# Performance work log

Hardware: AMD Instinct MI355X
Metric: run time of the kernel (lower is better)

The kernel has to match this reference:

```python
import jax, jax.numpy as jnp
import numpy as np

N_USERS = 100000
N_ITEMS = 100000
EMBED_DIM = 64
N_LAYERS = 3
NNZ = 1000000


def setup_inputs() -> dict:
    key = jax.random.key(0)
    k1, k2, k3, k4, k5 = jax.random.split(key, 5)
    N = N_USERS + N_ITEMS
    user_w = jax.random.normal(k1, (N_USERS, EMBED_DIM), dtype=jnp.float32) * 0.1
    item_w = jax.random.normal(k2, (N_ITEMS, EMBED_DIM), dtype=jnp.float32) * 0.1
    vals = jax.random.uniform(k3, (NNZ,), dtype=jnp.float32)
    rows = jax.random.randint(k4, (NNZ,), 0, N, dtype=jnp.int64 if jax.config.jax_enable_x64 else jnp.int32)
    cols = jax.random.randint(k5, (NNZ,), 0, N, dtype=jnp.int64 if jax.config.jax_enable_x64 else jnp.int32)
    return {"user_w": user_w, "item_w": item_w, "vals": vals, "rows": rows, "cols": cols}


def _spmm(vals, rows, cols, x, n):
    # sparse [n,n] COO  @  dense [n,d]  ->  [n,d]
    gathered = vals[:, None] * x[cols]          # [nnz, d]
    return jax.ops.segment_sum(gathered, rows, num_segments=n)


def reference(user_w, item_w, vals, rows, cols):
    # LightGCN-style propagation (SimGCL.propagate, perturb=False)
    n = user_w.shape[0] + item_w.shape[0]
    x = jnp.concatenate([user_w, item_w], axis=0)   # [N, d]
    acc = x                                         # running sum over layer stack
    for _ in range(N_LAYERS):
        x = _spmm(vals, rows, cols, x, n)
        acc = acc + x
    out = acc / jnp.asarray(N_LAYERS + 1, dtype=acc.dtype)  # mean over stacked embs
    return out[: user_w.shape[0]], out[user_w.shape[0]:]
```

## Files before the change

kernel.cpp:

```cpp
#include <hip/hip_runtime.h>
#include <hip/hip_bf16.h>
#include <hip/hip_fp16.h>

#define EMB 64
#define SCAN_CHUNK 1024
#define BSHIFT 11
#define BROWS (1 << BSHIFT)
#define NBMAX 128
#define TILE 4096

__device__ __forceinline__ float ld_elem(const void* p, long long i, int bf) {
    if (bf) return (float)((const __hip_bfloat16*)p)[i];
    return ((const float*)p)[i];
}

__global__ void hist_rows(const int* __restrict__ rows, int* __restrict__ counts, int nnz,
                          const unsigned short* __restrict__ v16, int* __restrict__ flag) {
    int tid = blockIdx.x * blockDim.x + threadIdx.x;
    int stride = gridDim.x * blockDim.x;
    for (int e = tid; e < nnz; e += stride) atomicAdd(&counts[rows[e]], 1);
    if (tid == 0) {
        int hits = 0;
        for (int i = 0; i < 256; ++i) {
            unsigned int hb = v16[i] >> 8;
            unsigned int ex = hb & 0x7F;
            if (hb < 0x80 && ex >= 0x30 && ex < 0x40) hits++;
        }
        *flag = (hits >= 200) ? 1 : 0;
    }
}

__global__ void scan_blocks(const int* __restrict__ in, int* __restrict__ excl,
                            int* __restrict__ blocksums, int n) {
    __shared__ int lds[256];
    int base = blockIdx.x * SCAN_CHUNK;
    int t = threadIdx.x;
    int c[4]; int s = 0;
    for (int k = 0; k < 4; ++k) {
        int i = base + t * 4 + k;
        c[k] = (i < n) ? in[i] : 0;
        s += c[k];
    }
    lds[t] = s;
    __syncthreads();
    for (int off = 1; off < 256; off <<= 1) {
        int v = lds[t];
        int add = (t >= off) ? lds[t - off] : 0;
        __syncthreads();
        lds[t] = v + add;
        __syncthreads();
    }
    int run = (t > 0) ? lds[t - 1] : 0;
    if (t == 255) blocksums[blockIdx.x] = lds[255];
    for (int k = 0; k < 4; ++k) {
        int i = base + t * 4 + k;
        if (i < n) excl[i] = run;
        run += c[k];
    }
}

__global__ void scan_fixup(int* __restrict__ excl, const int* __restrict__ bsums,
                           int* __restrict__ bcur, int n, int nrows, int nb) {
    __shared__ int lds[256];
    int t = threadIdx.x;
    lds[t] = (t < nb) ? bsums[t] : 0;
    __syncthreads();
    for (int off = 1; off < 256; off <<= 1) {
        int v = lds[t];
        int add = (t >= off) ? lds[t - off] : 0;
        __syncthreads();
        lds[t] = v + add;
        __syncthreads();
    }
    __syncthreads();
    int i = blockIdx.x * blockDim.x + threadIdx.x;
    if (i >= n) return;
    int b = i / SCAN_CHUNK;
    int v = excl[i] + (b > 0 ? lds[b - 1] : 0);
    excl[i] = v;
    if (i < nrows && (i & (BROWS - 1)) == 0) bcur[i >> BSHIFT] = v;
}

__global__ void bucket_scatter(const void* __restrict__ vals, const int* __restrict__ rows,
                               const int* __restrict__ cols, int* __restrict__ bcur,
                               float2* __restrict__ staged, int nnz, int nbuck,
                               const int* __restrict__ flagp) {
    __shared__ int hist[NBMAX];
    __shared__ int exb[NBMAX];
    __shared__ int gb[NBMAX];
    __shared__ int sc[NBMAX];
    __shared__ float2 st[TILE];
    __shared__ int bkt[TILE];
    int t = threadIdx.x;
    int bf = *flagp;

    for (int tile = blockIdx.x * TILE; tile < nnz; tile += gridDim.x * TILE) {
        int cnt = min(TILE, nnz - tile);
        for (int i = t; i < NBMAX; i += 256) hist[i] = 0;
        __syncthreads();

        int   myb[16], myo[16], mmeta[16];
        float mv[16];
#pragma unroll
        for (int k = 0; k < 16; ++k) {
            int i = tile + k * 256 + t;
            if (i < nnz && (k * 256 + t) < cnt) {
                int r = rows[i], c = cols[i];
                mv[k]    = ld_elem(vals, i, bf);
                myb[k]   = r >> BSHIFT;
                mmeta[k] = ((r & (BROWS - 1)) << 18) | c;
                myo[k]   = atomicAdd(&hist[myb[k]], 1);
            } else myb[k] = -1;
        }
        __syncthreads();

        if (t < NBMAX) sc[t] = hist[t];
        __syncthreads();
        for (int off = 1; off < NBMAX; off <<= 1) {
            int v = 0;
            if (t < NBMAX) { v = sc[t]; if (t >= off) v += sc[t - off]; }
            __syncthreads();
            if (t < NBMAX) sc[t] = v;
            __syncthreads();
        }
        if (t < NBMAX) {
            exb[t] = sc[t] - hist[t];
            if (t < nbuck && hist[t] > 0) gb[t] = atomicAdd(&bcur[t], hist[t]);
        }
        __syncthreads();

#pragma unroll
        for (int k = 0; k < 16; ++k) {
            if (myb[k] >= 0) {
                int p = exb[myb[k]] + myo[k];
                st[p]  = make_float2(mv[k], __int_as_float(mmeta[k]));
                bkt[p] = myb[k];
            }
        }
        __syncthreads();

        for (int p = t; p < cnt; p += 256) {
            int b = bkt[p];
            staged[gb[b] + (p - exb[b])] = st[p];
        }
        __syncthreads();
    }
}

__global__ void bucket_place(const int* __restrict__ row_ptr,
                             const float2* __restrict__ staged,
                             float2* __restrict__ edges, int nrows) {
    __shared__ int loffs[BROWS];
    int b = blockIdx.x;
    int rlo = b << BSHIFT;
    int rhi = min(rlo + BROWS, nrows);
    int nr  = rhi - rlo;
    int base = row_ptr[rlo];
    int end  = row_ptr[rhi];
    for (int i = threadIdx.x; i < nr; i += 256) loffs[i] = row_ptr[rlo + i] - base;
    __syncthreads();
    for (int p = base + threadIdx.x; p < end; p += 256) {
        float2 rec = staged[p];
        int meta = __float_as_int(rec.y);
        int lr = meta >> 18;
        int c  = meta & 0x3FFFF;
        int pos = atomicAdd(&loffs[lr], 1);
        edges[base + pos] = make_float2(rec.x, __int_as_float(c));
    }
}

__device__ __forceinline__ float4 ld4_x0(const void* uw, const void* iw,
                                         int n_user_elems, long long e, int bf) {
    const void* base = uw;
    if (e >= (long long)n_user_elems) { base = iw; e -= n_user_elems; }
    if (bf) {
        uint2 r = *reinterpret_cast<const uint2*>((const unsigned short*)base + e);
        return make_float4(__uint_as_float((r.x & 0xFFFFu) << 16),
                           __uint_as_float(r.x & 0xFFFF0000u),
                           __uint_as_float((r.y & 0xFFFFu) << 16),
                           __uint_as_float(r.y & 0xFFFF0000u));
    }
    return *reinterpret_cast<const float4*>((const float*)base + e);
}

__device__ __forceinline__ float4 ld4_f16(const __half* g, long long e) {
    uint2 r = *reinterpret_cast<const uint2*>(g + e);
    union { unsigned int u; __half2 h; } c0, c1;
    c0.u = r.x; c1.u = r.y;
    float2 f0 = __half22float2(c0.h), f1 = __half22float2(c1.h);
    return make_float4(f0.x, f0.y, f1.x, f1.y);
}

template <int GMODE, int OMODE>
__global__ void spmm_csr4(const int* __restrict__ row_ptr,
                          const float2* __restrict__ edges,
                          const void* __restrict__ uw, const void* __restrict__ iw,
                          int n_user_elems,
                          const __half* __restrict__ gin, void* __restrict__ gout,
                          int nrows, const int* __restrict__ flagp) {
    int tid  = blockIdx.x * blockDim.x + threadIdx.x;
    int wave = tid >> 6;
    int lane = threadIdx.x & 63;
    int g    = lane >> 4;
    int l    = lane & 15;
    int wid  = wave * 4 + g;
    if (wid >= nrows) return;
    int bf = *flagp;
    int beg = row_ptr[wid], end = row_ptr[wid + 1];
    float a0 = 0.f, a1 = 0.f, a2 = 0.f, a3 = 0.f;

#define GATHER(E, X) { \
        long long ce = (long long)__float_as_int((E).y) * EMB + l * 4; \
        if (GMODE == 0) X = ld4_x0(uw, iw, n_user_elems, ce, bf); \
        else            X = ld4_f16(gin, ce); }
#define ACC(E, X) { a0 += (E).x * (X).x; a1 += (E).x * (X).y; \
                    a2 += (E).x * (X).z; a3 += (E).x * (X).w; }

    int j = beg;
    for (; j + 4 <= end; j += 4) {
        float2 e0 = edges[j], e1 = edges[j + 1], e2 = edges[j + 2], e3 = edges[j + 3];
        float4 xa, xb, xc, xd;
        GATHER(e0, xa); GATHER(e1, xb); GATHER(e2, xc); GATHER(e3, xd);
        ACC(e0, xa); ACC(e1, xb); ACC(e2, xc); ACC(e3, xd);
    }
    if (j + 2 <= end) {
        float2 e0 = edges[j], e1 = edges[j + 1];
        float4 xa, xb;
        GATHER(e0, xa); GATHER(e1, xb);
        ACC(e0, xa); ACC(e1, xb);
        j += 2;
    }
    if (j < end) {
        float2 e0 = edges[j];
        float4 xa; GATHER(e0, xa);
        ACC(e0, xa);
    }
#undef GATHER
#undef ACC

    long long re = (long long)wid * EMB + l * 4;
    float4 x0v = ld4_x0(uw, iw, n_user_elems, re, bf);
    float o0 = x0v.x + a0, o1 = x0v.y + a1, o2 = x0v.z + a2, o3 = x0v.w + a3;

    if (OMODE == 1) {
        __half2 h01 = __floats2half2_rn(o0, o1);
        __half2 h23 = __floats2half2_rn(o2, o3);
        union { __half2 h; unsigned int u; } p0, p1;
        p0.h = h01; p1.h = h23;
        uint2 out; out.x = p0.u; out.y = p1.u;
        reinterpret_cast<uint2*>(gout)[re >> 2] = out;
    } else {
        o0 *= 0.25f; o1 *= 0.25f; o2 *= 0.25f; o3 *= 0.25f;
        if (bf) {
            __hip_bfloat16 b0 = (__hip_bfloat16)o0, b1 = (__hip_bfloat16)o1;
            __hip_bfloat16 b2 = (__hip_bfloat16)o2, b3 = (__hip_bfloat16)o3;
            unsigned short s0 = *reinterpret_cast<unsigned short*>(&b0);
            unsigned short s1 = *reinterpret_cast<unsigned short*>(&b1);
            unsigned short s2 = *reinterpret_cast<unsigned short*>(&b2);
            unsigned short s3 = *reinterpret_cast<unsigned short*>(&b3);
            uint2 out;
            out.x = (unsigned int)s0 | ((unsigned int)s1 << 16);
            out.y = (unsigned int)s2 | ((unsigned int)s3 << 16);
            reinterpret_cast<uint2*>(gout)[re >> 2] = out;
        } else {
            reinterpret_cast<float4*>(gout)[re >> 2] = make_float4(o0, o1, o2, o3);
        }
    }
}

extern "C" void kernel_launch(void* const* d_in, const int* in_sizes, int n_in,
                              void* d_out, int out_size, void* d_ws, size_t ws_size,
                              hipStream_t stream) {
    const void* uw   = d_in[0];
    const void* iw   = d_in[1];
    const void* vals = d_in[2];
    const int*  rows = (const int*)d_in[3];
    const int*  cols = (const int*)d_in[4];

    const int n_user = in_sizes[0];
    const int total  = in_sizes[0] + in_sizes[1];
    const int nnz    = in_sizes[2];
    const int nrows  = total / EMB;
    const int nbuck  = (nrows + BROWS - 1) >> BSHIFT;

    char* p = (char*)d_ws;
    auto alloc = [&](size_t bytes) { char* q = p; p += (bytes + 255) & ~(size_t)255; return q; };
    int*    flag    = (int*)   alloc(sizeof(int));
    int*    row_ptr = (int*)   alloc((size_t)(nrows + 1) * sizeof(int));
    int*    counts  = (int*)   alloc((size_t)(nrows + 1) * sizeof(int));
    int*    bcur    = (int*)   alloc(NBMAX * sizeof(int));
    int*    bsums   = (int*)   alloc(1024 * sizeof(int));
    float2* staged  = (float2*)alloc((size_t)nnz * sizeof(float2));
    float2* edges   = (float2*)alloc((size_t)nnz * sizeof(float2));
    size_t used = (size_t)(p - (char*)d_ws);
    size_t avail = (ws_size > used) ? ws_size - used : 0;

    const size_t g_f16 = (size_t)total * sizeof(__half);
    __half *g2, *g3;
    if (avail >= 2 * g_f16 + 512) { g2 = (__half*)alloc(g_f16); g3 = (__half*)alloc(g_f16); }
    else { g2 = (__half*)d_out; g3 = (__half*)alloc(g_f16); }

    hipMemsetAsync(counts, 0, (size_t)(nrows + 1) * sizeof(int), stream);
    const int hb = (nnz / 4 + 255) / 256;
    hist_rows<<<hb, 256, 0, stream>>>(rows, counts, nnz, (const unsigned short*)vals, flag);
    const int n_scan = nrows + 1;
    const int nb = (n_scan + SCAN_CHUNK - 1) / SCAN_CHUNK;
    scan_blocks<<<nb, 256, 0, stream>>>(counts, row_ptr, bsums, n_scan);
    scan_fixup<<<(n_scan + 255) / 256, 256, 0, stream>>>(row_ptr, bsums, bcur, n_scan, nrows, nb);

    const int ntiles = (nnz + TILE - 1) / TILE;
    bucket_scatter<<<ntiles, 256, 0, stream>>>(vals, rows, cols, bcur, staged, nnz, nbuck, flag);
    bucket_place<<<nbuck, 256, 0, stream>>>(row_ptr, staged, edges, nrows);

    const int nwaves = (nrows + 3) / 4;
    const int rb = (nwaves * 64 + 255) / 256;
    spmm_csr4<0, 1><<<rb, 256, 0, stream>>>(row_ptr, edges, uw, iw, n_user,
                                            nullptr, g2, nrows, flag);
    spmm_csr4<1, 1><<<rb, 256, 0, stream>>>(row_ptr, edges, uw, iw, n_user,
                                            g2, g3, nrows, flag);
    spmm_csr4<1, 3><<<rb, 256, 0, stream>>>(row_ptr, edges, uw, iw, n_user,
                                            g3, d_out, nrows, flag);
}
```

Before: 300.0 us.

## Build CSR from coarse bucket histogram and compute per-row offsets inside buckets

Swaps the per-row global-atomic histogram plus the two-kernel scan for a coarse per-bucket histogram kept in shared memory and a single-block scan. Per-row counts and the row_ptr prefix sum are now computed inside each bucket's block during the placement pass, from the staged metadata. This removes about 1M global atomics, a large memset and two scan launches, but each bucket block now makes two passes over its staged edges and runs a local scan. Only 98 bucket blocks do that work, so the placement stage may not fill the GPU.

New measurement: 272.1 us. -9.3%, faster.

```diff
diff --git a/kernel.cpp b/kernel.cpp
--- a/kernel.cpp
+++ b/kernel.cpp
@@ -3,7 +3,6 @@
 #include <hip/hip_fp16.h>
 
 #define EMB 64
-#define SCAN_CHUNK 1024
 #define BSHIFT 11
 #define BROWS (1 << BSHIFT)
 #define NBMAX 128
@@ -14,11 +13,39 @@
     return ((const float*)p)[i];
 }
 
-__global__ void hist_rows(const int* __restrict__ rows, int* __restrict__ counts, int nnz,
-                          const unsigned short* __restrict__ v16, int* __restrict__ flag) {
-    int tid = blockIdx.x * blockDim.x + threadIdx.x;
+__device__ __forceinline__ float4 ld4_x0(const void* uw, const void* iw,
+                                         int n_user_elems, long long e, int bf) {
+    const void* base = uw;
+    if (e >= (long long)n_user_elems) { base = iw; e -= n_user_elems; }
+    if (bf) {
+        uint2 r = *reinterpret_cast<const uint2*>((const unsigned short*)base + e);
+        return make_float4(__uint_as_float((r.x & 0xFFFFu) << 16),
+                           __uint_as_float(r.x & 0xFFFF0000u),
+                           __uint_as_float((r.y & 0xFFFFu) << 16),
+                           __uint_as_float(r.y & 0xFFFF0000u));
+    }
+    return *reinterpret_cast<const float4*>((const float*)base + e);
+}
+
+__device__ __forceinline__ float4 ld4_f16(const __half* g, long long e) {
+    uint2 r = *reinterpret_cast<const uint2*>(g + e);
+    union { unsigned int u; __half2 h; } c0, c1;
+    c0.u = r.x; c1.u = r.y;
+    float2 f0 = __half22float2(c0.h), f1 = __half22float2(c1.h);
+    return make_float4(f0.x, f0.y, f1.x, f1.y);
+}
+
+__global__ void hist_coarse(const int* __restrict__ rows, int* __restrict__ counts, int nnz,
+                            const unsigned short* __restrict__ v16, int* __restrict__ flag) {
+    __shared__ int h[NBMAX];
+    int t = threadIdx.x;
+    if (t < NBMAX) h[t] = 0;
+    __syncthreads();
+    int tid = blockIdx.x * blockDim.x + t;
     int stride = gridDim.x * blockDim.x;
-    for (int e = tid; e < nnz; e += stride) atomicAdd(&counts[rows[e]], 1);
+    for (int e = tid; e < nnz; e += stride) atomicAdd(&h[rows[e] >> BSHIFT], 1);
+    __syncthreads();
+    if (t < NBMAX) { int v = h[t]; if (v) atomicAdd(&counts[t], v); }
     if (tid == 0) {
         int hits = 0;
         for (int i = 0; i < 256; ++i) {
@@ -30,55 +57,22 @@
     }
 }
 
-__global__ void scan_blocks(const int* __restrict__ in, int* __restrict__ excl,
-                            int* __restrict__ blocksums, int n) {
-    __shared__ int lds[256];
-    int base = blockIdx.x * SCAN_CHUNK;
+__global__ void scan_coarse(const int* __restrict__ counts, int* __restrict__ cptr,
+                            int* __restrict__ bcur, int nb) {
+    __shared__ int lds[128];
     int t = threadIdx.x;
-    int c[4]; int s = 0;
-    for (int k = 0; k < 4; ++k) {
-        int i = base + t * 4 + k;
-        c[k] = (i < n) ? in[i] : 0;
-        s += c[k];
-    }
-    lds[t] = s;
-    __syncthreads();
-    for (int off = 1; off < 256; off <<= 1) {
-        int v = lds[t];
-        int add = (t >= off) ? lds[t - off] : 0;
-        __syncthreads();
-        lds[t] = v + add;
-        __syncthreads();
-    }
-    int run = (t > 0) ? lds[t - 1] : 0;
-    if (t == 255) blocksums[blockIdx.x] = lds[255];
-    for (int k = 0; k < 4; ++k) {
-        int i = base + t * 4 + k;
-        if (i < n) excl[i] = run;
-        run += c[k];
-    }
-}
-
-__global__ void scan_fixup(int* __restrict__ excl, const int* __restrict__ bsums,
-                           int* __restrict__ bcur, int n, int nrows, int nb) {
-    __shared__ int lds[256];
-    int t = threadIdx.x;
-    lds[t] = (t < nb) ? bsums[t] : 0;
-    __syncthreads();
-    for (int off = 1; off < 256; off <<= 1) {
-        int v = lds[t];
-        int add = (t >= off) ? lds[t - off] : 0;
-        __syncthreads();
-        lds[t] = v + add;
-        __syncthreads();
-    }
-    __syncthreads();
-    int i = blockIdx.x * blockDim.x + threadIdx.x;
-    if (i >= n) return;
-    int b = i / SCAN_CHUNK;
-    int v = excl[i] + (b > 0 ? lds[b - 1] : 0);
-    excl[i] = v;
-    if (i < nrows && (i & (BROWS - 1)) == 0) bcur[i >> BSHIFT] = v;
+    int v = (t < nb) ? counts[t] : 0;
+    lds[t] = v;
+    __syncthreads();
+    for (int off = 1; off < 128; off <<= 1) {
+        int x = lds[t];
+        int a = (t >= off) ? lds[t - off] : 0;
+        __syncthreads();
+        lds[t] = x + a;
+        __syncthreads();
+    }
+    if (t < nb) { int excl = lds[t] - v; cptr[t] = excl; bcur[t] = excl; }
+    if (t == 0) cptr[nb] = lds[127];
 }
 
 __global__ void bucket_scatter(const void* __restrict__ vals, const int* __restrict__ rows,
@@ -147,48 +141,57 @@
     }
 }
 
-__global__ void bucket_place(const int* __restrict__ row_ptr,
-                             const float2* __restrict__ staged,
-                             float2* __restrict__ edges, int nrows) {
-    __shared__ int loffs[BROWS];
+__global__ void bucket_csr(const int* __restrict__ cptr,
+                           const float2* __restrict__ staged,
+                           float2* __restrict__ edges,
+                           int* __restrict__ row_ptr, int nrows, int nbuck) {
+    __shared__ int rcnt[BROWS];
+    __shared__ int ssum[256];
     int b = blockIdx.x;
+    int t = threadIdx.x;
+    int cbeg = cptr[b], cend = cptr[b + 1];
     int rlo = b << BSHIFT;
-    int rhi = min(rlo + BROWS, nrows);
-    int nr  = rhi - rlo;
-    int base = row_ptr[rlo];
-    int end  = row_ptr[rhi];
-    for (int i = threadIdx.x; i < nr; i += 256) loffs[i] = row_ptr[rlo + i] - base;
-    __syncthreads();
-    for (int p = base + threadIdx.x; p < end; p += 256) {
-        float2 rec = staged[p];
+    int nr = min(BROWS, nrows - rlo);
+
+    for (int i = t; i < BROWS; i += 256) rcnt[i] = 0;
+    __syncthreads();
+
+    const int* sm = (const int*)staged;
+    for (int i = cbeg + t; i < cend; i += 256) {
+        int lr = (sm[2 * i + 1] >> 18) & (BROWS - 1);
+        atomicAdd(&rcnt[lr], 1);
+    }
+    __syncthreads();
+
+    int base = t * 8;
+    int loc[8]; int s = 0;
+#pragma unroll
+    for (int k = 0; k < 8; ++k) { loc[k] = rcnt[base + k]; s += loc[k]; }
+    ssum[t] = s;
+    __syncthreads();
+    for (int off = 1; off < 256; off <<= 1) {
+        int x = ssum[t];
+        int a = (t >= off) ? ssum[t - off] : 0;
+        __syncthreads();
+        ssum[t] = x + a;
+        __syncthreads();
+    }
+    int run = (t > 0) ? ssum[t - 1] : 0;
+#pragma unroll
+    for (int k = 0; k < 8; ++k) { int c = loc[k]; rcnt[base + k] = run; run += c; }
+    __syncthreads();
+
+    for (int i = t; i < nr; i += 256) row_ptr[rlo + i] = cbeg + rcnt[i];
+    if (b == nbuck - 1 && t == 0) row_ptr[nrows] = cend;
+
+    for (int i = cbeg + t; i < cend; i += 256) {
+        float2 rec = staged[i];
         int meta = __float_as_int(rec.y);
-        int lr = meta >> 18;
+        int lr = (meta >> 18) & (BROWS - 1);
         int c  = meta & 0x3FFFF;
-        int pos = atomicAdd(&loffs[lr], 1);
-        edges[base + pos] = make_float2(rec.x, __int_as_float(c));
-    }
-}
-
-__device__ __forceinline__ float4 ld4_x0(const void* uw, const void* iw,
-                                         int n_user_elems, long long e, int bf) {
-    const void* base = uw;
-    if (e >= (long long)n_user_elems) { base = iw; e -= n_user_elems; }
-    if (bf) {
-        uint2 r = *reinterpret_cast<const uint2*>((const unsigned short*)base + e);
-        return make_float4(__uint_as_float((r.x & 0xFFFFu) << 16),
-                           __uint_as_float(r.x & 0xFFFF0000u),
-                           __uint_as_float((r.y & 0xFFFFu) << 16),
-                           __uint_as_float(r.y & 0xFFFF0000u));
-    }
-    return *reinterpret_cast<const float4*>((const float*)base + e);
-}
-
-__device__ __forceinline__ float4 ld4_f16(const __half* g, long long e) {
-    uint2 r = *reinterpret_cast<const uint2*>(g + e);
-    union { unsigned int u; __half2 h; } c0, c1;
-    c0.u = r.x; c1.u = r.y;
-    float2 f0 = __half22float2(c0.h), f1 = __half22float2(c1.h);
-    return make_float4(f0.x, f0.y, f1.x, f1.y);
+        int pos = atomicAdd(&rcnt[lr], 1);
+        edges[cbeg + pos] = make_float2(rec.x, __int_as_float(c));
+    }
 }
 
 template <int GMODE, int OMODE>
@@ -286,10 +289,10 @@
     char* p = (char*)d_ws;
     auto alloc = [&](size_t bytes) { char* q = p; p += (bytes + 255) & ~(size_t)255; return q; };
     int*    flag    = (int*)   alloc(sizeof(int));
+    int*    counts  = (int*)   alloc(NBMAX * sizeof(int));
+    int*    cptr    = (int*)   alloc((NBMAX + 1) * sizeof(int));
+    int*    bcur    = (int*)   alloc(NBMAX * sizeof(int));
     int*    row_ptr = (int*)   alloc((size_t)(nrows + 1) * sizeof(int));
-    int*    counts  = (int*)   alloc((size_t)(nrows + 1) * sizeof(int));
-    int*    bcur    = (int*)   alloc(NBMAX * sizeof(int));
-    int*    bsums   = (int*)   alloc(1024 * sizeof(int));
     float2* staged  = (float2*)alloc((size_t)nnz * sizeof(float2));
     float2* edges   = (float2*)alloc((size_t)nnz * sizeof(float2));
     size_t used = (size_t)(p - (char*)d_ws);
@@ -300,17 +303,12 @@
     if (avail >= 2 * g_f16 + 512) { g2 = (__half*)alloc(g_f16); g3 = (__half*)alloc(g_f16); }
     else { g2 = (__half*)d_out; g3 = (__half*)alloc(g_f16); }
 
-    hipMemsetAsync(counts, 0, (size_t)(nrows + 1) * sizeof(int), stream);
-    const int hb = (nnz / 4 + 255) / 256;
-    hist_rows<<<hb, 256, 0, stream>>>(rows, counts, nnz, (const unsigned short*)vals, flag);
-    const int n_scan = nrows + 1;
-    const int nb = (n_scan + SCAN_CHUNK - 1) / SCAN_CHUNK;
-    scan_blocks<<<nb, 256, 0, stream>>>(counts, row_ptr, bsums, n_scan);
-    scan_fixup<<<(n_scan + 255) / 256, 256, 0, stream>>>(row_ptr, bsums, bcur, n_scan, nrows, nb);
-
+    hipMemsetAsync(counts, 0, NBMAX * sizeof(int), stream);
+    hist_coarse<<<120, 256, 0, stream>>>(rows, counts, nnz, (const unsigned short*)vals, flag);
+    scan_coarse<<<1, 128, 0, stream>>>(counts, cptr, bcur, nbuck);
     const int ntiles = (nnz + TILE - 1) / TILE;
     bucket_scatter<<<ntiles, 256, 0, stream>>>(vals, rows, cols, bcur, staged, nnz, nbuck, flag);
-    bucket_place<<<nbuck, 256, 0, stream>>>(row_ptr, staged, edges, nrows);
+    bucket_csr<<<nbuck, 256, 0, stream>>>(cptr, staged, edges, row_ptr, nrows, nbuck);
 
     const int nwaves = (nrows + 3) / 4;
     const int rb = (nwaves * 64 + 255) / 256;
```
